# Performance work log

Measured on AMD Instinct MI355X. Metric: run time of the kernel, lower is better.

## Reference

```python
import jax, jax.numpy as jnp
import numpy as np


def setup_inputs() -> dict:
    key = jax.random.key(0)
    k1, k2, k3 = jax.random.split(key, 3)
    N, M, H = 32768, 4096, 768
    fact = jax.random.normal(k1, (N, H), dtype=jnp.float32)
    elements_p = jax.random.normal(k2, (M, H), dtype=jnp.float32)
    # kaiming_uniform with a=sqrt(5) on [H,H]: bound = sqrt(6/((1+5)*H)) = 1/sqrt(H)
    bound = 1.0 / np.sqrt(H)
    weights = jax.random.uniform(k3, (H, H), dtype=jnp.float32, minval=-bound, maxval=bound)
    return {"fact": fact, "elements_p": elements_p, "weights": weights}


def reference(fact, elements_p, weights):
    # fact: [N,H], elements_p: [M,H], weights: [H,H]
    fact_Q = jnp.max(fact, axis=0, keepdims=True)                 # [1,H]
    f2e = (fact_Q @ weights) @ elements_p.T                        # [1,M]
    f2e = jax.nn.softmax(f2e, axis=-1)
    elements_p_ = jnp.sum(elements_p * f2e.T, axis=0, keepdims=True)  # [1,H]
    e2f = (fact @ weights) @ elements_p_.T                         # [N,1]
    e2f = jax.nn.softmax(e2f, axis=0)
    fact_ = jnp.sum(fact * e2f, axis=0, keepdims=True)             # [1,H]
    return (fact_, elements_p_)
```

## Files before the change

kernel.cpp:

```cpp
#include <hip/hip_runtime.h>
#include <math.h>


#define H 768
#define H4 192
#define PSTRIDE 772
#define ACC_OFF 4
#define NBLK 256
#define NTAIL 8
#define TAILB (NBLK - NTAIL)

__device__ __forceinline__ float wave_max(float x) {
#pragma unroll
  for (int o = 32; o; o >>= 1) x = fmaxf(x, __shfl_xor(x, o, 64));
  return x;
}
__device__ __forceinline__ float wave_sum(float x) {
#pragma unroll
  for (int o = 32; o; o >>= 1) x += __shfl_xor(x, o, 64);
  return x;
}
__device__ __forceinline__ float4 f4max(float4 a, float4 b) {
  return make_float4(fmaxf(a.x, b.x), fmaxf(a.y, b.y), fmaxf(a.z, b.z), fmaxf(a.w, b.w));
}

struct SMem {
  float4 sacc[8][H4];
  float sred[16];
};

__device__ __forceinline__ void stream_pass(const float4* __restrict__ X4,
                                            const float* __restrict__ wvec,
                                            float* __restrict__ part, int R,
                                            SMem& sm) {
  const int tid = threadIdx.x, lane = tid & 63, wv = tid >> 6;
  float4 wr[3];
#pragma unroll
  for (int j = 0; j < 3; ++j) wr[j] = ((const float4*)wvec)[lane + 64 * j];
  const int nw = NBLK * 8;
  const int gw = blockIdx.x * 8 + wv;
  const int rpw = (R + nw - 1) / nw;
  const int r0 = gw * rpw;
  const int r1 = min(R, r0 + rpw);
  float mrun = -INFINITY, l = 0.f;
  float4 acc[3];
#pragma unroll
  for (int j = 0; j < 3; ++j) acc[j] = make_float4(0.f, 0.f, 0.f, 0.f);
  for (int r = r0; r < r1; ++r) {
    const float4* row = X4 + (size_t)r * H4;
    float4 x[3];
    float s = 0.f;
#pragma unroll
    for (int j = 0; j < 3; ++j) {
      x[j] = row[lane + 64 * j];
      s = fmaf(x[j].x, wr[j].x, s);
      s = fmaf(x[j].y, wr[j].y, s);
      s = fmaf(x[j].z, wr[j].z, s);
      s = fmaf(x[j].w, wr[j].w, s);
    }
    s = wave_sum(s);
    const float mn = fmaxf(mrun, s);
    const float esc = __expf(mrun - mn);
    const float p = __expf(s - mn);
    l = fmaf(l, esc, p);
#pragma unroll
    for (int j = 0; j < 3; ++j) {
      acc[j].x = fmaf(acc[j].x, esc, p * x[j].x);
      acc[j].y = fmaf(acc[j].y, esc, p * x[j].y);
      acc[j].z = fmaf(acc[j].z, esc, p * x[j].z);
      acc[j].w = fmaf(acc[j].w, esc, p * x[j].w);
    }
    mrun = mn;
  }
  if (lane == 0) { sm.sred[wv] = mrun; sm.sred[8 + wv] = l; }
#pragma unroll
  for (int j = 0; j < 3; ++j) sm.sacc[wv][lane + 64 * j] = acc[j];
  __syncthreads();
  if (wv == 0) {
    float gm = -INFINITY;
#pragma unroll
    for (int w2 = 0; w2 < 8; ++w2) gm = fmaxf(gm, sm.sred[w2]);
    float fa[8];
    float L = 0.f;
#pragma unroll
    for (int w2 = 0; w2 < 8; ++w2) {
      const float lw = sm.sred[8 + w2];
      fa[w2] = (lw > 0.f) ? __expf(sm.sred[w2] - gm) : 0.f;
      L = fmaf(fa[w2], lw, L);
    }
    float* pb = part + (size_t)blockIdx.x * PSTRIDE;
#pragma unroll
    for (int j = 0; j < 3; ++j) {
      float4 a = make_float4(0.f, 0.f, 0.f, 0.f);
#pragma unroll
      for (int w2 = 0; w2 < 8; ++w2) {
        const float4 t = sm.sacc[w2][lane + 64 * j];
        a.x = fmaf(fa[w2], t.x, a.x);
        a.y = fmaf(fa[w2], t.y, a.y);
        a.z = fmaf(fa[w2], t.z, a.z);
        a.w = fmaf(fa[w2], t.w, a.w);
      }
      *(float4*)(pb + ACC_OFF + 4 * (lane + 64 * j)) = a;
    }
    if (lane == 0) { pb[0] = gm; pb[1] = L; }
  }
}

__global__ __launch_bounds__(192) void k_colmax_q(
    const float4* __restrict__ x4, float4* __restrict__ pmax4, int N,
    unsigned int* __restrict__ cnts, float* __restrict__ q,
    float* __restrict__ v, const float4* __restrict__ W4) {
  const int t = threadIdx.x;
  const int b = blockIdx.x;
  if (b == 0) {
    if (t < 8) cnts[t] = 0u;
    __threadfence();
#pragma unroll
    for (int j = 0; j < 4; ++j) { q[t + 192 * j] = 0.f; v[t + 192 * j] = 0.f; }
  }
  {
    float d = 0.f;
    const int base = b * 576;
#pragma unroll
    for (int j = 0; j < 3; ++j) {
      const float4 w = W4[base + t + 192 * j];
      d += w.x + w.y + w.z + w.w;
    }
    asm volatile("" ::"v"(d));
  }
  const int rpb = (N + NBLK - 1) / NBLK;
  const int n0 = b * rpb;
  float4 m = make_float4(-INFINITY, -INFINITY, -INFINITY, -INFINITY);
  for (int i = 0; i < rpb; i += 16) {
    float4 xr[16];
#pragma unroll
    for (int u = 0; u < 16; ++u) xr[u] = x4[(size_t)(n0 + i + u) * H4 + t];
#pragma unroll
    for (int u = 0; u < 16; ++u) m = f4max(m, xr[u]);
  }
  pmax4[(size_t)b * H4 + t] = m;

  __shared__ unsigned int s_rank;
  __syncthreads();
  if (t == 0) {
    __threadfence();
    s_rank = atomicAdd(&cnts[0], 1u);
  }
  __syncthreads();
  const unsigned int rank = s_rank;
  if (rank < (unsigned)TAILB) return;

  if (t == 0) {
    while (__hip_atomic_load(&cnts[0], __ATOMIC_ACQUIRE, __HIP_MEMORY_SCOPE_AGENT) <
           (unsigned)NBLK)
      __builtin_amdgcn_s_sleep(8);
  }
  __syncthreads();
  __threadfence();

  const int sl = (int)rank - TAILB;
  const int k0 = sl * 96;
  const int c4 = sl * 24;
  __shared__ float4 sq[8][24];
  __shared__ float sfQ[96];
  {
    const int col = t % 24;
    const int pg = t / 24;
    float4 m4 = make_float4(-INFINITY, -INFINITY, -INFINITY, -INFINITY);
#pragma unroll 8
    for (int i = 0; i < 32; ++i)
      m4 = f4max(m4, pmax4[(size_t)(pg + 8 * i) * H4 + c4 + col]);
    sq[pg][col] = m4;
  }
  __syncthreads();
  if (t < 24) {
    float4 s = sq[0][t];
#pragma unroll
    for (int g = 1; g < 8; ++g) s = f4max(s, sq[g][t]);
    ((float4*)sfQ)[t] = s;
  }
  __syncthreads();
  float4 acc = make_float4(0.f, 0.f, 0.f, 0.f);
#pragma unroll 8
  for (int kk = 0; kk < 96; ++kk) {
    const float f = sfQ[kk];
    const float4 w = W4[(size_t)(k0 + kk) * H4 + t];
    acc.x = fmaf(f, w.x, acc.x);
    acc.y = fmaf(f, w.y, acc.y);
    acc.z = fmaf(f, w.z, acc.z);
    acc.w = fmaf(f, w.w, acc.w);
  }
  atomicAdd(&q[4 * t + 0], acc.x);
  atomicAdd(&q[4 * t + 1], acc.y);
  atomicAdd(&q[4 * t + 2], acc.z);
  atomicAdd(&q[4 * t + 3], acc.w);
}

__global__ __launch_bounds__(512) void k_ep_comb(
    const float4* __restrict__ ep4, const float* __restrict__ q,
    float* __restrict__ pm, int M, const float4* __restrict__ W4,
    float4* __restrict__ out_ep, float* __restrict__ v,
    unsigned int* __restrict__ cnt) {
  const int tid = threadIdx.x;
  __shared__ SMem sm;
  stream_pass(ep4, q, pm, M, sm);

  __shared__ unsigned int s_rank;
  __syncthreads();
  if (tid == 0) {
    __threadfence();
    s_rank = atomicAdd(cnt, 1u);
  }
  __syncthreads();
  const unsigned int rank = s_rank;
  if (rank < (unsigned)TAILB) return;
  if (tid == 0) {
    while (__hip_atomic_load(cnt, __ATOMIC_ACQUIRE, __HIP_MEMORY_SCOPE_AGENT) <
           (unsigned)NBLK)
      __builtin_amdgcn_s_sleep(8);
  }
  __syncthreads();
  __threadfence();

  const int sl = (int)rank - TAILB;
  const int cb4 = sl * 24;
  const float* P = pm;
  __shared__ float tm[NBLK], tl[NBLK], te[NBLK];
  __shared__ float sgm, sLt4[4];
  __shared__ float4 sga[21][24];
  __shared__ float4 srr[24];
  if (tid < NBLK) {
    const float* pb = P + (size_t)tid * PSTRIDE;
    tm[tid] = pb[0];
    tl[tid] = pb[1];
  }
  __syncthreads();
  if (tid < 64) {
    float g = fmaxf(fmaxf(tm[tid], tm[tid + 64]), fmaxf(tm[tid + 128], tm[tid + 192]));
    g = wave_max(g);
    if (tid == 0) sgm = g;
  }
  __syncthreads();
  const float gm = sgm;
  if (tid < NBLK) te[tid] = (tl[tid] > 0.f) ? __expf(tm[tid] - gm) : 0.f;
  __syncthreads();
  if (tid < NBLK) {
    float x = te[tid] * tl[tid];
    x = wave_sum(x);
    if ((tid & 63) == 0) sLt4[tid >> 6] = x;
  }
  __syncthreads();
  const float inv = 1.f / (sLt4[0] + sLt4[1] + sLt4[2] + sLt4[3]);
  if (tid < 504) {
    const int c = tid % 24;
    const int pg = tid / 24;
    float4 a = make_float4(0.f, 0.f, 0.f, 0.f);
    for (int p = pg; p < NBLK; p += 21) {
      const float e = te[p];
      const float4 t4 = *(const float4*)(P + (size_t)p * PSTRIDE + ACC_OFF + 4 * (cb4 + c));
      a.x = fmaf(e, t4.x, a.x);
      a.y = fmaf(e, t4.y, a.y);
      a.z = fmaf(e, t4.z, a.z);
      a.w = fmaf(e, t4.w, a.w);
    }
    sga[pg][c] = a;
  }
  __syncthreads();
  if (tid < 24) {
    float4 s = sga[0][tid];
#pragma unroll
    for (int pg = 1; pg < 21; ++pg) {
      const float4 t4 = sga[pg][tid];
      s.x += t4.x; s.y += t4.y; s.z += t4.z; s.w += t4.w;
    }
    const float4 r = make_float4(s.x * inv, s.y * inv, s.z * inv, s.w * inv);
    out_ep[cb4 + tid] = r;
    srr[tid] = r;
  }
  __syncthreads();
  for (int i = tid; i < H; i += 512) {
    float s = 0.f;
#pragma unroll
    for (int c = 0; c < 24; ++c) {
      const float4 w = W4[(size_t)i * H4 + cb4 + c];
      const float4 r = srr[c];
      s = fmaf(w.x, r.x, fmaf(w.y, r.y, fmaf(w.z, r.z, fmaf(w.w, r.w, s))));
    }
    atomicAdd(&v[i], s);
  }
}

__global__ __launch_bounds__(512) void k_fact(const float4* __restrict__ X4,
                                              const float* __restrict__ v,
                                              float* __restrict__ pn,
                                              float* __restrict__ pn2, int R,
                                              unsigned int* __restrict__ cntA,
                                              unsigned int* __restrict__ cntB,
                                              float* __restrict__ outp) {
  const int tid = threadIdx.x, lane = tid & 63, wv = tid >> 6;
  __shared__ SMem sm;
  stream_pass(X4, v, pn, R, sm);

  __shared__ unsigned int s_rank;
  __syncthreads();
  if (tid == 0) {
    __threadfence();
    s_rank = atomicAdd(cntA, 1u);
  }
  __syncthreads();
  const unsigned int rank = s_rank;
  if (rank < (unsigned)(NBLK - 8)) return;

  if (tid == 0) {
    while (__hip_atomic_load(cntA, __ATOMIC_ACQUIRE, __HIP_MEMORY_SCOPE_AGENT) <
           (unsigned)NBLK)
      __builtin_amdgcn_s_sleep(8);
  }
  __syncthreads();
  __threadfence();

  const int slice = (int)rank - (NBLK - 8);
  const float* Pb = pn + (size_t)slice * 32 * PSTRIDE;
  __shared__ float s32m[32], s32l[32];
  if (tid < 32) {
    s32m[tid] = Pb[(size_t)tid * PSTRIDE];
    s32l[tid] = Pb[(size_t)tid * PSTRIDE + 1];
  }
  __syncthreads();
  float gms = -INFINITY;
#pragma unroll
  for (int b = 0; b < 32; ++b) gms = fmaxf(gms, s32m[b]);
  float4 a[3];
#pragma unroll
  for (int j = 0; j < 3; ++j) a[j] = make_float4(0.f, 0.f, 0.f, 0.f);
  for (int b = wv; b < 32; b += 8) {
    const float e = (s32l[b] > 0.f) ? __expf(s32m[b] - gms) : 0.f;
    const float4* pa = (const float4*)(Pb + (size_t)b * PSTRIDE + ACC_OFF);
#pragma unroll
    for (int j = 0; j < 3; ++j) {
      const float4 t = pa[lane + 64 * j];
      a[j].x = fmaf(e, t.x, a[j].x);
      a[j].y = fmaf(e, t.y, a[j].y);
      a[j].z = fmaf(e, t.z, a[j].z);
      a[j].w = fmaf(e, t.w, a[j].w);
    }
  }
  float lc = 0.f;
  if (tid < 32) lc = ((s32l[tid] > 0.f) ? __expf(s32m[tid] - gms) : 0.f) * s32l[tid];
  lc = wave_sum(lc);
  __syncthreads();
#pragma unroll
  for (int j = 0; j < 3; ++j) sm.sacc[wv][lane + 64 * j] = a[j];
  if (tid == 0) sm.sred[0] = lc;
  __syncthreads();
  float* qb = pn2 + (size_t)slice * PSTRIDE;
  if (tid < H4) {
    float4 s = sm.sacc[0][tid];
#pragma unroll
    for (int w2 = 1; w2 < 8; ++w2) {
      const float4 t = sm.sacc[w2][tid];
      s.x += t.x; s.y += t.y; s.z += t.z; s.w += t.w;
    }
    *(float4*)(qb + ACC_OFF + 4 * tid) = s;
  }
  if (tid == 0) { qb[0] = gms; qb[1] = sm.sred[0]; }

  __syncthreads();
  __shared__ unsigned int s_r2;
  if (tid == 0) {
    __threadfence();
    s_r2 = atomicAdd(cntB, 1u);
  }
  __syncthreads();
  if (s_r2 != 7u) return;
  __threadfence();

  __shared__ float s8m[8], s8l[8];
  if (tid < 8) {
    s8m[tid] = pn2[(size_t)tid * PSTRIDE];
    s8l[tid] = pn2[(size_t)tid * PSTRIDE + 1];
  }
  __syncthreads();
  float gm = -INFINITY;
#pragma unroll
  for (int k = 0; k < 8; ++k) gm = fmaxf(gm, s8m[k]);
  float Lt = 0.f;
#pragma unroll
  for (int k = 0; k < 8; ++k)
    Lt += ((s8l[k] > 0.f) ? __expf(s8m[k] - gm) : 0.f) * s8l[k];
  float4 b[3];
  {
    const int k = wv;
    const float e = (s8l[k] > 0.f) ? __expf(s8m[k] - gm) : 0.f;
    const float4* pa = (const float4*)(pn2 + (size_t)k * PSTRIDE + ACC_OFF);
#pragma unroll
    for (int j = 0; j < 3; ++j) {
      const float4 t = pa[lane + 64 * j];
      b[j] = make_float4(e * t.x, e * t.y, e * t.z, e * t.w);
    }
  }
  __syncthreads();
#pragma unroll
  for (int j = 0; j < 3; ++j) sm.sacc[wv][lane + 64 * j] = b[j];
  __syncthreads();
  if (tid < H4) {
    float4 s = sm.sacc[0][tid];
#pragma unroll
    for (int w2 = 1; w2 < 8; ++w2) {
      const float4 t = sm.sacc[w2][tid];
      s.x += t.x; s.y += t.y; s.z += t.z; s.w += t.w;
    }
    const float inv = 1.f / Lt;
    ((float4*)outp)[tid] = make_float4(s.x * inv, s.y * inv, s.z * inv, s.w * inv);
  }
}

extern "C" void kernel_launch(void* const* d_in, const int* in_sizes, int n_in,
                              void* d_out, int out_size, void* d_ws, size_t ws_size,
                              hipStream_t stream) {
  const float4* fact4 = (const float4*)d_in[0];
  const float4* ep4   = (const float4*)d_in[1];
  const float4* W4    = (const float4*)d_in[2];
  float* out = (float*)d_out;
  const int N = in_sizes[0] / H;
  const int M = in_sizes[1] / H;

  float* wsf = (float*)d_ws;
  unsigned int* cnts = (unsigned int*)d_ws;
  float* q     = wsf + 8;
  float* v     = wsf + 776;
  float* pmaxf = wsf + 1544;
  float* pm    = wsf + 198152;
  float* pn    = wsf + 395784;
  float* pn2   = wsf + 593416;

  k_colmax_q<<<NBLK, 192, 0, stream>>>(fact4, (float4*)pmaxf, N, cnts, q, v, W4);
  k_ep_comb<<<NBLK, 512, 0, stream>>>(ep4, q, pm, M, W4, (float4*)(out + H), v, cnts + 1);
  k_fact<<<NBLK, 512, 0, stream>>>(fact4, v, pn, pn2, N, cnts + 2, cnts + 3, out);
}
```

Before: 246.4 us.

## Widen column-max kernel to 512 threads with wave-per-row streaming and LDS reduction

The column-max pass over fact now runs 8 waves per block instead of 3. Each wave reads whole rows, two rows at a time, and keeps two accumulator sets. A shared-memory reduction across the waves then produces the per-block partial max. The aim is more memory-level parallelism per CU on this bandwidth-bound 100MB read. The cost is an extra LDS reduction and a barrier, and the tail-phase code gains guards so only the first 192 threads take part.

```diff
diff --git a/kernel.cpp b/kernel.cpp
--- a/kernel.cpp
+++ b/kernel.cpp
@@ -106,39 +106,65 @@
   }
 }
 
-__global__ __launch_bounds__(192) void k_colmax_q(
+__global__ __launch_bounds__(512) void k_colmax_q(
     const float4* __restrict__ x4, float4* __restrict__ pmax4, int N,
     unsigned int* __restrict__ cnts, float* __restrict__ q,
     float* __restrict__ v, const float4* __restrict__ W4) {
-  const int t = threadIdx.x;
+  const int t = threadIdx.x, lane = t & 63, wv = t >> 6;
   const int b = blockIdx.x;
+  __shared__ float4 sacc[8][H4];
   if (b == 0) {
     if (t < 8) cnts[t] = 0u;
     __threadfence();
 #pragma unroll
-    for (int j = 0; j < 4; ++j) { q[t + 192 * j] = 0.f; v[t + 192 * j] = 0.f; }
+    for (int j = 0; j < 2; ++j) {
+      const int i = t + 512 * j;
+      if (i < H) { q[i] = 0.f; v[i] = 0.f; }
+    }
   }
   {
     float d = 0.f;
     const int base = b * 576;
-#pragma unroll
-    for (int j = 0; j < 3; ++j) {
-      const float4 w = W4[base + t + 192 * j];
-      d += w.x + w.y + w.z + w.w;
+    const float4 w0 = W4[base + t];
+    d += w0.x + w0.y + w0.z + w0.w;
+    if (t < 64) {
+      const float4 w1 = W4[base + 512 + t];
+      d += w1.x + w1.y + w1.z + w1.w;
     }
     asm volatile("" ::"v"(d));
   }
   const int rpb = (N + NBLK - 1) / NBLK;
   const int n0 = b * rpb;
-  float4 m = make_float4(-INFINITY, -INFINITY, -INFINITY, -INFINITY);
-  for (int i = 0; i < rpb; i += 16) {
-    float4 xr[16];
-#pragma unroll
-    for (int u = 0; u < 16; ++u) xr[u] = x4[(size_t)(n0 + i + u) * H4 + t];
-#pragma unroll
-    for (int u = 0; u < 16; ++u) m = f4max(m, xr[u]);
-  }
-  pmax4[(size_t)b * H4 + t] = m;
+  float4 a0[3], a1[3];
+#pragma unroll
+  for (int j = 0; j < 3; ++j) {
+    a0[j] = make_float4(-INFINITY, -INFINITY, -INFINITY, -INFINITY);
+    a1[j] = a0[j];
+  }
+  for (int r = n0 + wv; r < n0 + rpb; r += 16) {
+    const float4* rowA = x4 + (size_t)r * H4;
+    const float4* rowB = x4 + (size_t)(r + 8) * H4;
+    float4 xa[3], xb[3];
+#pragma unroll
+    for (int j = 0; j < 3; ++j) {
+      xa[j] = rowA[lane + 64 * j];
+      xb[j] = rowB[lane + 64 * j];
+    }
+#pragma unroll
+    for (int j = 0; j < 3; ++j) {
+      a0[j] = f4max(a0[j], xa[j]);
+      a1[j] = f4max(a1[j], xb[j]);
+    }
+  }
+#pragma unroll
+  for (int j = 0; j < 3; ++j) sacc[wv][lane + 64 * j] = f4max(a0[j], a1[j]);
+  __syncthreads();
+  if (t < H4) {
+    float4 mm = sacc[0][t];
+#pragma unroll
+    for (int w2 = 1; w2 < 8; ++w2) mm = f4max(mm, sacc[w2][t]);
+    pmax4[(size_t)b * H4 + t] = mm;
+  }
 
   __shared__ unsigned int s_rank;
   __syncthreads();
@@ -163,7 +189,7 @@
   const int c4 = sl * 24;
   __shared__ float4 sq[8][24];
   __shared__ float sfQ[96];
-  {
+  if (t < 192) {
     const int col = t % 24;
     const int pg = t / 24;
     float4 m4 = make_float4(-INFINITY, -INFINITY, -INFINITY, -INFINITY);
@@ -180,20 +206,22 @@
     ((float4*)sfQ)[t] = s;
   }
   __syncthreads();
-  float4 acc = make_float4(0.f, 0.f, 0.f, 0.f);
+  if (t < H4) {
+    float4 acc = make_float4(0.f, 0.f, 0.f, 0.f);
 #pragma unroll 8
-  for (int kk = 0; kk < 96; ++kk) {
-    const float f = sfQ[kk];
-    const float4 w = W4[(size_t)(k0 + kk) * H4 + t];
-    acc.x = fmaf(f, w.x, acc.x);
-    acc.y = fmaf(f, w.y, acc.y);
-    acc.z = fmaf(f, w.z, acc.z);
-    acc.w = fmaf(f, w.w, acc.w);
-  }
-  atomicAdd(&q[4 * t + 0], acc.x);
-  atomicAdd(&q[4 * t + 1], acc.y);
-  atomicAdd(&q[4 * t + 2], acc.z);
-  atomicAdd(&q[4 * t + 3], acc.w);
+    for (int kk = 0; kk < 96; ++kk) {
+      const float f = sfQ[kk];
+      const float4 w = W4[(size_t)(k0 + kk) * H4 + t];
+      acc.x = fmaf(f, w.x, acc.x);
+      acc.y = fmaf(f, w.y, acc.y);
+      acc.z = fmaf(f, w.z, acc.z);
+      acc.w = fmaf(f, w.w, acc.w);
+    }
+    atomicAdd(&q[4 * t + 0], acc.x);
+    atomicAdd(&q[4 * t + 1], acc.y);
+    atomicAdd(&q[4 * t + 2], acc.z);
+    atomicAdd(&q[4 * t + 3], acc.w);
+  }
 }
 
 __global__ __launch_bounds__(512) void k_ep_comb(
@@ -434,7 +462,7 @@
   float* pn    = wsf + 395784;
   float* pn2   = wsf + 593416;
 
-  k_colmax_q<<<NBLK, 192, 0, stream>>>(fact4, (float4*)pmaxf, N, cnts, q, v, W4);
+  k_colmax_q<<<NBLK, 512, 0, stream>>>(fact4, (float4*)pmaxf, N, cnts, q, v, W4);
   k_ep_comb<<<NBLK, 512, 0, stream>>>(ep4, q, pm, M, W4, (float4*)(out + H), v, cnts + 1);
   k_fact<<<NBLK, 512, 0, stream>>>(fact4, v, pn, pn2, N, cnts + 2, cnts + 3, out);
 }
```

Measured after the change: 253.2 us. 2.8% more time.
